# Optimization experiments

Hardware: AMD Instinct MI355X
Metric: run time of the kernel (lower is better)

Reference implementation:

```python
import jax, jax.numpy as jnp
import numpy as np

N, E, D, H, K = 100000, 1600000, 512, 256, 64


def setup_inputs() -> dict:
    key = jax.random.key(0)
    ks = jax.random.split(key, 8)
    x = jax.random.normal(ks[0], (N, D), dtype=jnp.float32)
    edge_index = jax.random.randint(ks[1], (2, E), 0, N, dtype=jnp.int64)
    W1 = jax.random.normal(ks[2], (D, H), dtype=jnp.float32) / np.sqrt(D)
    b1 = jnp.zeros((H,), dtype=jnp.float32)
    W2 = jax.random.normal(ks[3], (H, H), dtype=jnp.float32) / np.sqrt(H)
    b2 = jnp.zeros((H,), dtype=jnp.float32)
    Wk = jax.random.normal(ks[4], (H, K), dtype=jnp.float32) / np.sqrt(H)
    log_tau = jnp.array(np.log(1.0), dtype=jnp.float32)
    return {"x": x, "edge_index": edge_index, "W1": W1, "b1": b1,
            "W2": W2, "b2": b2, "Wk": Wk, "log_tau": log_tau}


def _gcn_norm(edge_index, n):
    # add self-loops, compute sym-normalized edge weights (PyG GCNConv default)
    loop = jnp.arange(n, dtype=edge_index.dtype)
    src = jnp.concatenate([edge_index[0], loop])
    dst = jnp.concatenate([edge_index[1], loop])
    deg = jax.ops.segment_sum(jnp.ones_like(dst, dtype=jnp.float32), dst, num_segments=n)
    dinv = jnp.where(deg > 0, jax.lax.rsqrt(deg), 0.0)
    norm = dinv[src] * dinv[dst]  # [E+N]
    return src, dst, norm


def _gcn_conv(h, W, b, src, dst, norm, n):
    hw = h @ W                      # dense GEMM [n, out]
    msg = hw[src] * norm[:, None]   # gather + scale
    out = jax.ops.segment_sum(msg, dst, num_segments=n)  # scatter-add
    return out + b


def reference(x, edge_index, W1, b1, W2, b2, Wk, log_tau):
    n = x.shape[0]
    src, dst, norm = _gcn_norm(edge_index, n)
    h = jax.nn.relu(_gcn_conv(x, W1, b1, src, dst, norm, n))
    h = _gcn_conv(h, W2, b2, src, dst, norm, n)
    logits = h @ Wk                 # [n, K]
    tau = jnp.exp(log_tau)
    S = jax.nn.softmax(logits / tau, axis=-1)
    return (S, logits)
```

## Files before the change

### kernel.cpp

```cpp
#include <hip/hip_runtime.h>

typedef unsigned short u16;
typedef unsigned int u32;

__device__ __forceinline__ float bfl(u32 u) { union { u32 i; float f; } v; v.i = u << 16; return v.f; }
__device__ __forceinline__ float bfh(u32 u) { union { u32 i; float f; } v; v.i = u & 0xffff0000u; return v.f; }
__device__ __forceinline__ float bf2f(u16 u) { union { u32 i; float f; } v; v.i = ((u32)u) << 16; return v.f; }
__device__ __forceinline__ u16 f2bf(float f) {
    union { float f; u32 i; } v; v.f = f;
    u32 r = v.i + 0x7fffu + ((v.i >> 16) & 1u);
    return (u16)(r >> 16);
}
__device__ __forceinline__ u32 pk2bf(float lo, float hi) {
    u32 r;
    asm("v_cvt_pk_bf16_f32 %0, %1, %2" : "=v"(r) : "v"(lo), "v"(hi));
    return r;
}

typedef const __attribute__((address_space(1))) unsigned int* gas_u32;
typedef __attribute__((address_space(3))) unsigned int* las_u32;
__device__ __forceinline__ void async_cp16(const void* g, void* l) {
    __builtin_amdgcn_global_load_lds((gas_u32)g, (las_u32)l, 16, 0, 0);
}

__global__ void k_detect(const u32* __restrict__ xw, const int* __restrict__ eiw,
                         const void* __restrict__ ltau, int* __restrict__ flags,
                         int* __restrict__ bcount,
                         int xwords, int E, int nb) {
    __shared__ int cf32, ci64nz;
    if (threadIdx.x == 0) { cf32 = 0; ci64nz = 0; }
    __syncthreads();
    int t = threadIdx.x;
    for (int i = t; i < nb; i += 256) bcount[i] = 0;
    int xs = xwords / 256;
    u32 w = xw[(size_t)t * xs];
    int e = (int)((w >> 23) & 0xFFu);
    if (e >= 100 && e <= 140) atomicAdd(&cf32, 1);
    int es = E / 256;
    int hw = eiw[2 * (size_t)t * es + 1];
    if (hw != 0) atomicAdd(&ci64nz, 1);
    __syncthreads();
    if (t == 0) {
        int f32 = (cf32 >= 192) ? 1 : 0;
        flags[0] = f32;
        flags[1] = (ci64nz == 0) ? 1 : 0;
        ((float*)flags)[2] = f32 ? ((const float*)ltau)[0] : bf2f(((const u16*)ltau)[0]);
    }
}

__global__ __launch_bounds__(256) void k_edges_count(const int* __restrict__ ei,
                                                     int* __restrict__ src, int* __restrict__ dst,
                                                     int* __restrict__ bcount,
                                                     int e, int nb, const int* __restrict__ flags) {
    __shared__ int h[1024];
    int t = threadIdx.x;
    for (int i = t; i < nb; i += 256) h[i] = 0;
    __syncthreads();
    const int i64 = flags[1];
    int chunk = (e + gridDim.x - 1) / gridDim.x;
    int beg = blockIdx.x * chunk;
    int end = beg + chunk; if (end > e) end = e;
    for (int i = beg + t; i < end; i += 256) {
        int s, d;
        if (i64) { s = ei[2 * i]; d = ei[2 * (e + i)]; }
        else     { s = ei[i];     d = ei[e + i]; }
        src[i] = s; dst[i] = d;
        atomicAdd(&h[d >> 7], 1);
    }
    __syncthreads();
    for (int i = t; i < nb; i += 256) { int v = h[i]; if (v) atomicAdd(&bcount[i], v); }
}

__global__ __launch_bounds__(1024) void k_bscan(const int* __restrict__ bcount, int* __restrict__ bbase,
                                                int* __restrict__ bcursor, int nb) {
    int t = threadIdx.x;
    int per = (nb + 1023) >> 10;
    int b0 = t * per;
    int ls[8];
    int s = 0;
#pragma unroll
    for (int j = 0; j < 8; j++) {
        int v = 0;
        if (j < per && b0 + j < nb) v = bcount[b0 + j];
        ls[j] = v; s += v;
    }
    int lane = t & 63, w = t >> 6;
    int inc = s;
    for (int d = 1; d < 64; d <<= 1) { int u = __shfl_up(inc, d); if (lane >= d) inc += u; }
    __shared__ int wsum[16];
    __shared__ int gtot;
    if (lane == 63) wsum[w] = inc;
    __syncthreads();
    if (t == 0) { int a = 0; for (int i = 0; i < 16; i++) { int x = wsum[i]; wsum[i] = a; a += x; } gtot = a; }
    __syncthreads();
    int base = wsum[w] + inc - s;
#pragma unroll
    for (int j = 0; j < 8; j++) {
        if (j < per && b0 + j < nb) { bbase[b0 + j] = base; bcursor[b0 + j] = base; base += ls[j]; }
    }
    if (t == 0) bbase[nb] = gtot;
}

__global__ __launch_bounds__(256) void k_bscatter(const int* __restrict__ src, const int* __restrict__ dst,
                                                  int* __restrict__ bcursor, u32* __restrict__ ebuf,
                                                  int e, int nb) {
    __shared__ int h[1024];
    __shared__ int lbase[1024];
    int t = threadIdx.x;
    for (int i = t; i < nb; i += 256) h[i] = 0;
    __syncthreads();
    int chunk = (e + gridDim.x - 1) / gridDim.x;
    int beg = blockIdx.x * chunk;
    int end = beg + chunk; if (end > e) end = e;
    for (int i = beg + t; i < end; i += 256) atomicAdd(&h[dst[i] >> 7], 1);
    __syncthreads();
    for (int i = t; i < nb; i += 256) {
        int v = h[i];
        lbase[i] = v ? atomicAdd(&bcursor[i], v) : 0;
        h[i] = 0;
    }
    __syncthreads();
    for (int i = beg + t; i < end; i += 256) {
        int d = dst[i];
        int b = d >> 7;
        int p = lbase[b] + atomicAdd(&h[b], 1);
        ebuf[p] = ((u32)(d & 127) << 25) | (u32)src[i];
    }
}

__global__ __launch_bounds__(256) void k_bcsr(const u32* __restrict__ ebuf, const int* __restrict__ bbase,
                                              int* __restrict__ row_ptr, float* __restrict__ dinv,
                                              int* __restrict__ col, int n, int nb, int e) {
    __shared__ int hist[128], sc[128], cur[128];
    int b = blockIdx.x, t = threadIdx.x;
    if (t < 128) hist[t] = 0;
    __syncthreads();
    int beg = bbase[b], end = bbase[b + 1];
    for (int j = beg + t; j < end; j += 256) atomicAdd(&hist[ebuf[j] >> 25], 1);
    __syncthreads();
    if (t < 128) sc[t] = hist[t];
    __syncthreads();
    for (int d = 1; d < 128; d <<= 1) {
        int v = 0;
        if (t < 128 && t >= d) v = sc[t - d];
        __syncthreads();
        if (t < 128) sc[t] += v;
        __syncthreads();
    }
    if (t < 128) {
        int node = (b << 7) + t;
        if (node < n) {
            int ex = sc[t] - hist[t];
            row_ptr[node] = beg + ex;
            dinv[node] = rsqrtf((float)(hist[t] + 1));
            cur[t] = ex;
        }
    }
    if (b == 0 && t == 0) row_ptr[n] = e;
    __syncthreads();
    for (int j = beg + t; j < end; j += 256) {
        u32 ev = ebuf[j];
        int dl = (int)(ev >> 25);
        int p = atomicAdd(&cur[dl], 1);
        col[beg + p] = (int)(ev & 0x1FFFFFFu);
    }
}

__global__ void k_transpose_flex(const void* __restrict__ in, u16* __restrict__ out,
                                 int R, int C, const int* __restrict__ flags) {
    int idx = blockIdx.x * 256 + threadIdx.x;
    if (idx >= R * C) return;
    u16 v = flags[0] ? f2bf(((const float*)in)[idx]) : ((const u16*)in)[idx];
    int r = idx / C, c = idx % C;
    out[(size_t)c * R + r] = v;
}

typedef __bf16 bf16x8 __attribute__((ext_vector_type(8)));
typedef float floatx4 __attribute__((ext_vector_type(4)));

template <int WROWS, int WCOLS, int TM, int TN, int MODE, bool AFLEX, bool OFLEX>
__global__ __launch_bounds__(WROWS * WCOLS * 64, 4)
void k_gemm_bt(const void* __restrict__ A,
               const u16* __restrict__ Bt,
               void* __restrict__ C,
               const float* __restrict__ dinv,
               const int* __restrict__ flags,
               long long obase,
               int M, int Nd, int Kd) {
    constexpr int THREADS = WROWS * WCOLS * 64;
    constexpr int BM = WROWS * TM * 16;
    constexpr int BN = WCOLS * TN * 16;
    constexpr int BK = 32;
    __shared__ u16 SMEM[2 * (BM + BN) * BK];
    auto As = (u16(*)[BM][BK])SMEM;
    auto Bs = (u16(*)[BN][BK])(SMEM + 2 * BM * BK);
    const int af32 = AFLEX ? flags[0] : 0;
    const int of32 = OFLEX ? flags[0] : 0;
    const int tid = threadIdx.x;
    const int m0 = blockIdx.y * BM;
    const int n0 = blockIdx.x * BN;
    const int lane = tid & 63;
    const int wave = tid >> 6;
    const int wm = wave / WCOLS;
    const int wn = wave % WCOLS;
    const int mrow = lane & 15;
    const int quad = lane >> 4;

    floatx4 acc[TM][TN];
#pragma unroll
    for (int i = 0; i < TM; i++)
#pragma unroll
        for (int j = 0; j < TN; j++) { floatx4 z = {0.f, 0.f, 0.f, 0.f}; acc[i][j] = z; }

    auto stage = [&](int kk, int buf) {
        if (AFLEX && af32) {
#pragma unroll
            for (int idx = tid * 8; idx < BM * BK; idx += THREADS * 8) {
                int r = idx >> 5, k = idx & 31;
                int gr = m0 + r;
                u32 t4[4] = {0, 0, 0, 0};
                if (gr < M) {
                    const float* ap = (const float*)A + (size_t)gr * Kd + kk + k;
                    float4 f0 = *(const float4*)ap;
                    float4 f1 = *(const float4*)(ap + 4);
                    t4[0] = pk2bf(f0.x, f0.y); t4[1] = pk2bf(f0.z, f0.w);
                    t4[2] = pk2bf(f1.x, f1.y); t4[3] = pk2bf(f1.z, f1.w);
                }
                *(int4*)&As[buf][r][k] = *(const int4*)t4;
            }
#pragma unroll
            for (int idx = tid * 8; idx < BN * BK; idx += THREADS * 8) {
                int r = idx >> 5, k = idx & 31;
                int4 v = *(const int4*)(Bt + (size_t)(n0 + r) * Kd + kk + k);
                *(int4*)&Bs[buf][r][k] = v;
            }
        } else {
#pragma unroll
            for (int idx = tid * 8; idx < BM * BK; idx += THREADS * 8) {
                int r = idx >> 5, k = idx & 31;
                int gr = m0 + r;
                if (gr >= M) gr = M - 1;
                async_cp16((const u16*)A + (size_t)gr * Kd + kk + k, &As[buf][r][k]);
            }
#pragma unroll
            for (int idx = tid * 8; idx < BN * BK; idx += THREADS * 8) {
                int r = idx >> 5, k = idx & 31;
                async_cp16(Bt + (size_t)(n0 + r) * Kd + kk + k, &Bs[buf][r][k]);
            }
        }
    };

    const int steps = Kd / BK;
    stage(0, 0);
    for (int s = 0; s < steps; s++) {
        __syncthreads();
        if (s + 1 < steps) stage((s + 1) * BK, (s + 1) & 1);
        const int b = s & 1;
        bf16x8 af[TM], bfr[TN];
#pragma unroll
        for (int i = 0; i < TM; i++)
            af[i] = *(const bf16x8*)&As[b][wm * TM * 16 + i * 16 + mrow][quad * 8];
#pragma unroll
        for (int j = 0; j < TN; j++)
            bfr[j] = *(const bf16x8*)&Bs[b][wn * TN * 16 + j * 16 + mrow][quad * 8];
#pragma unroll
        for (int i = 0; i < TM; i++)
#pragma unroll
            for (int j = 0; j < TN; j++)
                acc[i][j] = __builtin_amdgcn_mfma_f32_16x16x32_bf16(af[i], bfr[j], acc[i][j], 0, 0, 0);
    }

    if (MODE == 2) {
        float inv_tau = __expf(-((const float*)flags)[2]);
        float* Ct = (float*)SMEM;
        __syncthreads();
#pragma unroll
        for (int i = 0; i < TM; i++)
#pragma unroll
            for (int r = 0; r < 4; r++) {
                int row = i * 16 + quad * 4 + r;
                Ct[row * 64 + wn * 16 + mrow] = acc[i][0][r];
            }
        __syncthreads();
        for (int r16 = 0; r16 < 16; r16++) {
            int row = r16 * 4 + wave;
            float raw = Ct[row * 64 + lane];
            float xv = raw * inv_tau;
            float mx = xv;
            for (int d = 32; d; d >>= 1) mx = fmaxf(mx, __shfl_xor(mx, d));
            float ev = __expf(xv - mx);
            float sm = ev;
            for (int d = 32; d; d >>= 1) sm += __shfl_xor(sm, d);
            float rr = ev / sm;
            long long grow = m0 + row;
            if (grow < M) {
                long long si = grow * 64 + lane;
                if (of32) { ((float*)C)[si] = rr; ((float*)C)[obase + si] = raw; }
                else      { ((u16*)C)[si] = f2bf(rr); ((u16*)C)[obase + si] = f2bf(raw); }
            }
        }
        return;
    }

#pragma unroll
    for (int i = 0; i < TM; i++) {
#pragma unroll
        for (int r = 0; r < 4; r++) {
            int grow = m0 + wm * TM * 16 + i * 16 + quad * 4 + r;
            if (grow < M) {
                float scale = (MODE == 0) ? dinv[grow] : 1.0f;
#pragma unroll
                for (int j = 0; j < TN; j++) {
                    int gcol = n0 + wn * TN * 16 + j * 16 + mrow;
                    float val = acc[i][j][r] * scale;
                    long long cidx = obase + (long long)grow * Nd + gcol;
                    if (OFLEX && of32) ((float*)C)[cidx] = val;
                    else               ((u16*)C)[cidx] = f2bf(val);
                }
            }
        }
    }
}

__global__ __launch_bounds__(256) void k_agg(const u16* __restrict__ g, u16* __restrict__ out,
                                             const int* __restrict__ row_ptr,
                                             const int* __restrict__ col,
                                             const float* __restrict__ dinv,
                                             const void* __restrict__ bias,
                                             const int* __restrict__ flags,
                                             int n, int do_relu) {
    int gw = (int)((blockIdx.x * 256 + threadIdx.x) >> 6);
    int lane = threadIdx.x & 63;
    int half = lane >> 5;
    int l = lane & 31;
    const u16* gp = g + (size_t)l * 8;
    float b0, b1, b2, b3, b4, b5, b6, b7;
    if (flags[0]) {
        const float4* bp = (const float4*)bias;
        float4 q0 = bp[2 * l], q1 = bp[2 * l + 1];
        b0 = q0.x; b1 = q0.y; b2 = q0.z; b3 = q0.w;
        b4 = q1.x; b5 = q1.y; b6 = q1.z; b7 = q1.w;
    } else {
        uint4 bv = ((const uint4*)bias)[l];
        b0 = bfl(bv.x); b1 = bfh(bv.x); b2 = bfl(bv.y); b3 = bfh(bv.y);
        b4 = bfl(bv.z); b5 = bfh(bv.z); b6 = bfl(bv.w); b7 = bfh(bv.w);
    }
    int w1 = gw * 4 + 4; if (w1 > n) w1 = n;
    for (int wid = gw * 4; wid < w1; wid++) {
        float a0 = 0.f, a1 = 0.f, a2 = 0.f, a3 = 0.f, a4 = 0.f, a5 = 0.f, a6 = 0.f, a7 = 0.f;
        if (half == 0) {
            uint4 rv = *(const uint4*)(gp + (size_t)wid * 256);
            a0 += bfl(rv.x); a1 += bfh(rv.x); a2 += bfl(rv.y); a3 += bfh(rv.y);
            a4 += bfl(rv.z); a5 += bfh(rv.z); a6 += bfl(rv.w); a7 += bfh(rv.w);
        }
        int beg = row_ptr[wid], end = row_ptr[wid + 1];
        for (int base = beg; base < end; base += 64) {
            int m = end - base; if (m > 64) m = 64;
            int ci = (base + lane < end) ? col[base + lane] : 0;
            int j = 0;
            for (; j + 16 <= m; j += 16) {
                uint4 v[8];
#pragma unroll
                for (int q = 0; q < 8; q++) {
                    int s = __shfl(ci, j + 2 * q + half);
                    v[q] = *(const uint4*)(gp + (size_t)s * 256);
                }
#pragma unroll
                for (int q = 0; q < 8; q++) {
                    a0 += bfl(v[q].x); a1 += bfh(v[q].x);
                    a2 += bfl(v[q].y); a3 += bfh(v[q].y);
                    a4 += bfl(v[q].z); a5 += bfh(v[q].z);
                    a6 += bfl(v[q].w); a7 += bfh(v[q].w);
                }
            }
            for (; j < m; j += 2) {
                int idx = j + half;
                int s = __shfl(ci, idx < m ? idx : j);
                uint4 v = *(const uint4*)(gp + (size_t)s * 256);
                if (idx < m) {
                    a0 += bfl(v.x); a1 += bfh(v.x); a2 += bfl(v.y); a3 += bfh(v.y);
                    a4 += bfl(v.z); a5 += bfh(v.z); a6 += bfl(v.w); a7 += bfh(v.w);
                }
            }
        }
        a0 += __shfl_xor(a0, 32); a1 += __shfl_xor(a1, 32);
        a2 += __shfl_xor(a2, 32); a3 += __shfl_xor(a3, 32);
        a4 += __shfl_xor(a4, 32); a5 += __shfl_xor(a5, 32);
        a6 += __shfl_xor(a6, 32); a7 += __shfl_xor(a7, 32);
        if (half == 0) {
            float dv = dinv[wid];
            float c0 = a0 * dv + b0, c1 = a1 * dv + b1, c2 = a2 * dv + b2, c3 = a3 * dv + b3;
            float c4 = a4 * dv + b4, c5 = a5 * dv + b5, c6 = a6 * dv + b6, c7 = a7 * dv + b7;
            if (do_relu) {
                c0 = fmaxf(c0, 0.f); c1 = fmaxf(c1, 0.f); c2 = fmaxf(c2, 0.f); c3 = fmaxf(c3, 0.f);
                c4 = fmaxf(c4, 0.f); c5 = fmaxf(c5, 0.f); c6 = fmaxf(c6, 0.f); c7 = fmaxf(c7, 0.f);
            }
            uint4 o;
            o.x = (u32)f2bf(c0) | ((u32)f2bf(c1) << 16);
            o.y = (u32)f2bf(c2) | ((u32)f2bf(c3) << 16);
            o.z = (u32)f2bf(c4) | ((u32)f2bf(c5) << 16);
            o.w = (u32)f2bf(c6) | ((u32)f2bf(c7) << 16);
            *(uint4*)(out + (size_t)wid * 256 + (size_t)l * 8) = o;
        }
    }
}

extern "C" void kernel_launch(void* const* d_in, const int* in_sizes, int n_in,
                              void* d_out, int out_size, void* d_ws, size_t ws_size,
                              hipStream_t stream) {
    const void* x    = d_in[0];
    const int*  ei   = (const int*)d_in[1];
    const void* W1   = d_in[2];
    const void* b1   = d_in[3];
    const void* W2   = d_in[4];
    const void* b2   = d_in[5];
    const void* Wk   = d_in[6];
    const void* ltau = d_in[7];
    const int D = 512, H = 256, K = 64;
    const int N = in_sizes[0] / D;
    const int E = in_sizes[1] / 2;
    const long long NK = (long long)N * K;
    const int nb = (N + 127) >> 7;

    u16* g = (u16*)d_ws;
    u16* h = g + (size_t)N * H;
    int* flags = (int*)(h + (size_t)N * H);
    int* srcv = (int*)g;
    int* dstv = srcv + E;
    u32* ebuf = (u32*)(dstv + E);

    size_t ooff = 0;
    char* wsbase = (char*)(flags + 64);
    auto oalloc = [&](size_t bytes) -> char* {
        char* p = wsbase + ooff;
        ooff += (bytes + 255) & ~(size_t)255;
        return p;
    };
    int*   col     = (int*)oalloc((size_t)E * 4);
    float* dinv    = (float*)oalloc((size_t)N * 4);
    int*   row_ptr = (int*)oalloc((size_t)(N + 1) * 4);
    int*   bcount  = (int*)oalloc((size_t)nb * 4);
    int*   bbase   = (int*)oalloc((size_t)(nb + 1) * 4);
    int*   bcursor = (int*)oalloc((size_t)nb * 4);
    u16*   W1t     = (u16*)oalloc((size_t)D * H * 2);
    u16*   W2t     = (u16*)oalloc((size_t)H * H * 2);
    u16*   Wkt     = (u16*)oalloc((size_t)H * K * 2);

    auto g256 = [](long long n) { return (int)((n + 255) / 256); };

    k_detect<<<1, 256, 0, stream>>>((const u32*)x, ei, ltau, flags, bcount, in_sizes[0] / 2, E, nb);
    k_edges_count<<<256, 256, 0, stream>>>(ei, srcv, dstv, bcount, E, nb, flags);
    k_bscan<<<1, 1024, 0, stream>>>(bcount, bbase, bcursor, nb);
    k_bscatter<<<256, 256, 0, stream>>>(srcv, dstv, bcursor, ebuf, E, nb);
    k_bcsr<<<nb, 256, 0, stream>>>(ebuf, bbase, row_ptr, dinv, col, N, nb, E);

    k_transpose_flex<<<g256((long long)D * H), 256, 0, stream>>>(W1, W1t, D, H, flags);
    k_transpose_flex<<<g256((long long)H * H), 256, 0, stream>>>(W2, W2t, H, H, flags);
    k_transpose_flex<<<g256((long long)H * K), 256, 0, stream>>>(Wk, Wkt, H, K, flags);

    const int m64 = (N + 63) / 64;
    const long long aggw = ((long long)N + 3) / 4;
    k_gemm_bt<1, 4, 4, 4, 0, true, false>
        <<<dim3(1, m64), 256, 0, stream>>>(x, W1t, g, dinv, flags, 0, N, H, D);
    k_agg<<<g256(aggw * 64), 256, 0, stream>>>(g, h, row_ptr, col, dinv, b1, flags, N, 1);
    k_gemm_bt<1, 4, 4, 4, 0, false, false>
        <<<dim3(1, m64), 256, 0, stream>>>(h, W2t, g, dinv, flags, 0, N, H, H);
    k_agg<<<g256(aggw * 64), 256, 0, stream>>>(g, h, row_ptr, col, dinv, b2, flags, N, 0);
    k_gemm_bt<1, 4, 4, 1, 2, false, true>
        <<<dim3(1, m64), 256, 0, stream>>>(h, Wkt, d_out, dinv, flags, NK, N, K, H);
}
```

Measured before the change: 725.9 us.

## Assign one wavefront per node in aggregation and widen second GEMM tiles

After: 711.0 us. 1.02x faster.

```diff
diff --git a/kernel.cpp b/kernel.cpp
--- a/kernel.cpp
+++ b/kernel.cpp
@@ -329,79 +329,77 @@
                                              const void* __restrict__ bias,
                                              const int* __restrict__ flags,
                                              int n, int do_relu) {
-    int gw = (int)((blockIdx.x * 256 + threadIdx.x) >> 6);
+    int wid = (int)((blockIdx.x * 256 + threadIdx.x) >> 6);
     int lane = threadIdx.x & 63;
+    if (wid >= n) return;
     int half = lane >> 5;
     int l = lane & 31;
     const u16* gp = g + (size_t)l * 8;
-    float b0, b1, b2, b3, b4, b5, b6, b7;
-    if (flags[0]) {
-        const float4* bp = (const float4*)bias;
-        float4 q0 = bp[2 * l], q1 = bp[2 * l + 1];
-        b0 = q0.x; b1 = q0.y; b2 = q0.z; b3 = q0.w;
-        b4 = q1.x; b5 = q1.y; b6 = q1.z; b7 = q1.w;
-    } else {
-        uint4 bv = ((const uint4*)bias)[l];
-        b0 = bfl(bv.x); b1 = bfh(bv.x); b2 = bfl(bv.y); b3 = bfh(bv.y);
-        b4 = bfl(bv.z); b5 = bfh(bv.z); b6 = bfl(bv.w); b7 = bfh(bv.w);
-    }
-    int w1 = gw * 4 + 4; if (w1 > n) w1 = n;
-    for (int wid = gw * 4; wid < w1; wid++) {
-        float a0 = 0.f, a1 = 0.f, a2 = 0.f, a3 = 0.f, a4 = 0.f, a5 = 0.f, a6 = 0.f, a7 = 0.f;
-        if (half == 0) {
-            uint4 rv = *(const uint4*)(gp + (size_t)wid * 256);
-            a0 += bfl(rv.x); a1 += bfh(rv.x); a2 += bfl(rv.y); a3 += bfh(rv.y);
-            a4 += bfl(rv.z); a5 += bfh(rv.z); a6 += bfl(rv.w); a7 += bfh(rv.w);
-        }
-        int beg = row_ptr[wid], end = row_ptr[wid + 1];
-        for (int base = beg; base < end; base += 64) {
-            int m = end - base; if (m > 64) m = 64;
-            int ci = (base + lane < end) ? col[base + lane] : 0;
-            int j = 0;
-            for (; j + 16 <= m; j += 16) {
-                uint4 v[8];
-#pragma unroll
-                for (int q = 0; q < 8; q++) {
-                    int s = __shfl(ci, j + 2 * q + half);
-                    v[q] = *(const uint4*)(gp + (size_t)s * 256);
-                }
-#pragma unroll
-                for (int q = 0; q < 8; q++) {
-                    a0 += bfl(v[q].x); a1 += bfh(v[q].x);
-                    a2 += bfl(v[q].y); a3 += bfh(v[q].y);
-                    a4 += bfl(v[q].z); a5 += bfh(v[q].z);
-                    a6 += bfl(v[q].w); a7 += bfh(v[q].w);
-                }
-            }
-            for (; j < m; j += 2) {
-                int idx = j + half;
-                int s = __shfl(ci, idx < m ? idx : j);
-                uint4 v = *(const uint4*)(gp + (size_t)s * 256);
-                if (idx < m) {
-                    a0 += bfl(v.x); a1 += bfh(v.x); a2 += bfl(v.y); a3 += bfh(v.y);
-                    a4 += bfl(v.z); a5 += bfh(v.z); a6 += bfl(v.w); a7 += bfh(v.w);
-                }
-            }
-        }
-        a0 += __shfl_xor(a0, 32); a1 += __shfl_xor(a1, 32);
-        a2 += __shfl_xor(a2, 32); a3 += __shfl_xor(a3, 32);
-        a4 += __shfl_xor(a4, 32); a5 += __shfl_xor(a5, 32);
-        a6 += __shfl_xor(a6, 32); a7 += __shfl_xor(a7, 32);
-        if (half == 0) {
-            float dv = dinv[wid];
-            float c0 = a0 * dv + b0, c1 = a1 * dv + b1, c2 = a2 * dv + b2, c3 = a3 * dv + b3;
-            float c4 = a4 * dv + b4, c5 = a5 * dv + b5, c6 = a6 * dv + b6, c7 = a7 * dv + b7;
-            if (do_relu) {
-                c0 = fmaxf(c0, 0.f); c1 = fmaxf(c1, 0.f); c2 = fmaxf(c2, 0.f); c3 = fmaxf(c3, 0.f);
-                c4 = fmaxf(c4, 0.f); c5 = fmaxf(c5, 0.f); c6 = fmaxf(c6, 0.f); c7 = fmaxf(c7, 0.f);
-            }
-            uint4 o;
-            o.x = (u32)f2bf(c0) | ((u32)f2bf(c1) << 16);
-            o.y = (u32)f2bf(c2) | ((u32)f2bf(c3) << 16);
-            o.z = (u32)f2bf(c4) | ((u32)f2bf(c5) << 16);
-            o.w = (u32)f2bf(c6) | ((u32)f2bf(c7) << 16);
-            *(uint4*)(out + (size_t)wid * 256 + (size_t)l * 8) = o;
-        }
+    float a0 = 0.f, a1 = 0.f, a2 = 0.f, a3 = 0.f, a4 = 0.f, a5 = 0.f, a6 = 0.f, a7 = 0.f;
+    if (half == 0) {
+        uint4 rv = *(const uint4*)(gp + (size_t)wid * 256);
+        a0 += bfl(rv.x); a1 += bfh(rv.x); a2 += bfl(rv.y); a3 += bfh(rv.y);
+        a4 += bfl(rv.z); a5 += bfh(rv.z); a6 += bfl(rv.w); a7 += bfh(rv.w);
+    }
+    int beg = row_ptr[wid], end = row_ptr[wid + 1];
+    for (int base = beg; base < end; base += 64) {
+        int m = end - base; if (m > 64) m = 64;
+        int ci = (base + lane < end) ? col[base + lane] : 0;
+        int j = 0;
+        for (; j + 16 <= m; j += 16) {
+            uint4 v[8];
+#pragma unroll
+            for (int q = 0; q < 8; q++) {
+                int s = __shfl(ci, j + 2 * q + half);
+                v[q] = *(const uint4*)(gp + (size_t)s * 256);
+            }
+#pragma unroll
+            for (int q = 0; q < 8; q++) {
+                a0 += bfl(v[q].x); a1 += bfh(v[q].x);
+                a2 += bfl(v[q].y); a3 += bfh(v[q].y);
+                a4 += bfl(v[q].z); a5 += bfh(v[q].z);
+                a6 += bfl(v[q].w); a7 += bfh(v[q].w);
+            }
+        }
+        for (; j < m; j += 2) {
+            int idx = j + half;
+            int s = __shfl(ci, idx < m ? idx : j);
+            uint4 v = *(const uint4*)(gp + (size_t)s * 256);
+            if (idx < m) {
+                a0 += bfl(v.x); a1 += bfh(v.x); a2 += bfl(v.y); a3 += bfh(v.y);
+                a4 += bfl(v.z); a5 += bfh(v.z); a6 += bfl(v.w); a7 += bfh(v.w);
+            }
+        }
+    }
+    a0 += __shfl_xor(a0, 32); a1 += __shfl_xor(a1, 32);
+    a2 += __shfl_xor(a2, 32); a3 += __shfl_xor(a3, 32);
+    a4 += __shfl_xor(a4, 32); a5 += __shfl_xor(a5, 32);
+    a6 += __shfl_xor(a6, 32); a7 += __shfl_xor(a7, 32);
+    if (half == 0) {
+        float dv = dinv[wid];
+        float b0, b1, b2, b3, b4, b5, b6, b7;
+        if (flags[0]) {
+            const float4* bp = (const float4*)bias;
+            float4 q0 = bp[2 * l], q1 = bp[2 * l + 1];
+            b0 = q0.x; b1 = q0.y; b2 = q0.z; b3 = q0.w;
+            b4 = q1.x; b5 = q1.y; b6 = q1.z; b7 = q1.w;
+        } else {
+            uint4 bv = ((const uint4*)bias)[l];
+            b0 = bfl(bv.x); b1 = bfh(bv.x); b2 = bfl(bv.y); b3 = bfh(bv.y);
+            b4 = bfl(bv.z); b5 = bfh(bv.z); b6 = bfl(bv.w); b7 = bfh(bv.w);
+        }
+        a0 = a0 * dv + b0; a1 = a1 * dv + b1; a2 = a2 * dv + b2; a3 = a3 * dv + b3;
+        a4 = a4 * dv + b4; a5 = a5 * dv + b5; a6 = a6 * dv + b6; a7 = a7 * dv + b7;
+        if (do_relu) {
+            a0 = fmaxf(a0, 0.f); a1 = fmaxf(a1, 0.f); a2 = fmaxf(a2, 0.f); a3 = fmaxf(a3, 0.f);
+            a4 = fmaxf(a4, 0.f); a5 = fmaxf(a5, 0.f); a6 = fmaxf(a6, 0.f); a7 = fmaxf(a7, 0.f);
+        }
+        uint4 o;
+        o.x = (u32)f2bf(a0) | ((u32)f2bf(a1) << 16);
+        o.y = (u32)f2bf(a2) | ((u32)f2bf(a3) << 16);
+        o.z = (u32)f2bf(a4) | ((u32)f2bf(a5) << 16);
+        o.w = (u32)f2bf(a6) | ((u32)f2bf(a7) << 16);
+        *(uint4*)(out + (size_t)wid * 256 + (size_t)l * 8) = o;
     }
 }
 
@@ -459,13 +457,13 @@
     k_transpose_flex<<<g256((long long)H * K), 256, 0, stream>>>(Wk, Wkt, H, K, flags);
 
     const int m64 = (N + 63) / 64;
-    const long long aggw = ((long long)N + 3) / 4;
+    const int m128 = (N + 127) / 128;
     k_gemm_bt<1, 4, 4, 4, 0, true, false>
         <<<dim3(1, m64), 256, 0, stream>>>(x, W1t, g, dinv, flags, 0, N, H, D);
-    k_agg<<<g256(aggw * 64), 256, 0, stream>>>(g, h, row_ptr, col, dinv, b1, flags, N, 1);
-    k_gemm_bt<1, 4, 4, 4, 0, false, false>
-        <<<dim3(1, m64), 256, 0, stream>>>(h, W2t, g, dinv, flags, 0, N, H, H);
-    k_agg<<<g256(aggw * 64), 256, 0, stream>>>(g, h, row_ptr, col, dinv, b2, flags, N, 0);
+    k_agg<<<g256((long long)N * 64), 256, 0, stream>>>(g, h, row_ptr, col, dinv, b1, flags, N, 1);
+    k_gemm_bt<2, 4, 4, 4, 0, false, false>
+        <<<dim3(1, m128), 512, 0, stream>>>(h, W2t, g, dinv, flags, 0, N, H, H);
+    k_agg<<<g256((long long)N * 64), 256, 0, stream>>>(g, h, row_ptr, col, dinv, b2, flags, N, 0);
     k_gemm_bt<1, 4, 4, 1, 2, false, true>
         <<<dim3(1, m64), 256, 0, stream>>>(h, Wkt, d_out, dinv, flags, NK, N, K, H);
 }
```
